# Kernel optimization log

Hardware: AMD Instinct MI355X
Metric: run time of the kernel (lower is better)

The kernel has to match this reference:

```python
import jax, jax.numpy as jnp
import numpy as np
import math

D_MODEL = 1024
NUM_HEADS = 16
D_HEAD = D_MODEL // NUM_HEADS          # 64
N_FREQ = D_HEAD // 2 + 1               # 33 rfft bins
COMPRESSION_RATIO = 0.5


def setup_inputs() -> dict:
    key = jax.random.key(0)
    k_x, k_qkv, k_out, k_b, k_m = jax.random.split(key, 5)
    B, S = 2, 2048
    x = jax.random.normal(k_x, (B, S, D_MODEL), dtype=jnp.float32)
    # Linear weights stored as [in, out] (torch Linear uses [out, in]; math identical).
    w_qkv = jax.random.normal(k_qkv, (D_MODEL, 3 * D_MODEL), dtype=jnp.float32) / math.sqrt(D_MODEL)
    w_out = jax.random.normal(k_out, (D_MODEL, D_MODEL), dtype=jnp.float32) / math.sqrt(D_MODEL)
    b_out = jax.random.normal(k_b, (D_MODEL,), dtype=jnp.float32) * 0.01
    # Learned per-frequency-bin mask logits of AdaptiveFrequencyMask(d_state=d_head).
    # Initialized around logit(compression_ratio) with small noise.
    init_logit = math.log(COMPRESSION_RATIO / (1.0 - COMPRESSION_RATIO))
    mask_logits = init_logit + 0.1 * jax.random.normal(k_m, (N_FREQ,), dtype=jnp.float32)
    return {"x": x, "w_qkv": w_qkv, "w_out": w_out, "b_out": b_out, "mask_logits": mask_logits}


def _spectral_filter(t, mask):
    # rfft over d_head dim, apply learned soft mask, inverse rfft.  t: [B,H,S,dh]
    tf = jnp.fft.rfft(t, axis=-1)          # [B,H,S,N_FREQ] complex
    tf = tf * mask                          # broadcast real mask over bins
    return jnp.fft.irfft(tf, n=t.shape[-1], axis=-1).astype(t.dtype)


def reference(x, w_qkv, w_out, b_out, mask_logits):
    B, S, D = x.shape
    H, dh = NUM_HEADS, D_HEAD
    qkv = x @ w_qkv                                         # [B,S,3D]
    q, k, v = jnp.split(qkv, 3, axis=-1)
    # [B,S,D] -> [B,H,S,dh]
    to_heads = lambda t: t.reshape(B, S, H, dh).transpose(0, 2, 1, 3)
    q, k, v = to_heads(q), to_heads(k), to_heads(v)
    mask = jax.nn.sigmoid(mask_logits)                      # [N_FREQ]
    q = _spectral_filter(q, mask)
    k = _spectral_filter(k, mask)
    scores = jnp.einsum('bhqd,bhkd->bhqk', q, k) / math.sqrt(dh)
    attn = jax.nn.softmax(scores, axis=-1)                  # dropout p=0 (eval)
    out = jnp.einsum('bhqk,bhkd->bhqd', attn, v)
    out = out.transpose(0, 2, 1, 3).reshape(B, S, D)
    return out @ w_out + b_out
```

## Files before the change

kernel.cpp:

```cpp
#include <hip/hip_runtime.h>

#define S_LEN 2048
#define NH    16
#define DH    64
#define DM    1024
#define NQKV  3072

typedef __attribute__((ext_vector_type(8))) __bf16 bf16x8;
typedef __attribute__((ext_vector_type(4))) float  f32x4;
typedef unsigned short ushort_t;

static __device__ __forceinline__ unsigned short bf16b(float f) {
  return __builtin_bit_cast(unsigned short, (__bf16)f);
}

static __device__ __forceinline__ float exp2v(float x) {
  return __builtin_amdgcn_exp2f(x);
}

static __device__ __forceinline__ bf16x8 pack8(float4 f0, float4 f1) {
  uint4 v;
  v.x = ((unsigned)bf16b(f0.y) << 16) | bf16b(f0.x);
  v.y = ((unsigned)bf16b(f0.w) << 16) | bf16b(f0.z);
  v.z = ((unsigned)bf16b(f1.y) << 16) | bf16b(f1.x);
  v.w = ((unsigned)bf16b(f1.w) << 16) | bf16b(f1.z);
  return __builtin_bit_cast(bf16x8, v);
}

static __device__ __forceinline__ void glds16(const void* g, void* l) {
  __builtin_amdgcn_global_load_lds((const __attribute__((address_space(1))) unsigned int*)g,
                                   (__attribute__((address_space(3))) unsigned int*)l, 16, 0, 0);
}

#define OFF_WT  65536ull
#define OFF_WOT 6356992ull
#define OFF_Q   8454144ull
#define OFF_K   16842752ull
#define OFF_V   25231360ull
#define OFF_AO  33619968ull

__global__ __launch_bounds__(256) void k_fold(const float* __restrict__ wqkv,
                                              const float* __restrict__ logits,
                                              unsigned short* __restrict__ Wt) {
  __shared__ float msk[33];
  __shared__ float Kd[64];
  __shared__ __align__(16) unsigned short Fb[64][72];
  int t = threadIdx.x;
  if (t < 33) msk[t] = 1.0f / (1.0f + __expf(-logits[t]));
  __syncthreads();
  if (t < 64) {
    float acc = msk[0];
    #pragma unroll
    for (int f = 1; f < 32; ++f) {
      int r = (f * t) & 63;
      acc += 2.0f * msk[f] * __cosf((float)r * (6.28318530717958647692f / 64.0f));
    }
    acc += msk[32] * ((t & 1) ? -1.0f : 1.0f);
    Kd[t] = acc * (1.0f / 64.0f);
  }
  __syncthreads();
  for (int idx = t; idx < 4096; idx += 256) {
    int j = idx >> 6, i = idx & 63;
    Fb[j][i] = bf16b(Kd[(j - i) & 63]);
  }
  __syncthreads();

  int lane = t & 63, w = t >> 6;
  int m16 = lane & 15, quad = lane >> 4;
  int kx = blockIdx.x, yy = blockIdx.y;
  int which = yy >> 4, h = yy & 15;
  int base = which * 1024 + h * 64;

  bf16x8 af0 = *(const bf16x8*)(&Fb[w * 16 + m16][quad * 8]);
  bf16x8 af1 = *(const bf16x8*)(&Fb[w * 16 + m16][32 + quad * 8]);

  f32x4 acc[8] = {};
  #pragma unroll 2
  for (int n = 0; n < 8; ++n) {
    const float* Wg = wqkv + (size_t)(kx * 128 + n * 16 + m16) * NQKV + base + quad * 8;
    float4 a0 = *(const float4*)(Wg);
    float4 a1 = *(const float4*)(Wg + 4);
    float4 b0 = *(const float4*)(Wg + 32);
    float4 b1 = *(const float4*)(Wg + 36);
    acc[n] = __builtin_amdgcn_mfma_f32_16x16x32_bf16(af0, pack8(a0, a1), acc[n], 0, 0, 0);
    acc[n] = __builtin_amdgcn_mfma_f32_16x16x32_bf16(af1, pack8(b0, b1), acc[n], 0, 0, 0);
  }
  float sc = (which == 0) ? 0.18033688011112042f : 1.0f;
  #pragma unroll
  for (int n = 0; n < 8; ++n) {
    #pragma unroll
    for (int r = 0; r < 4; ++r) {
      int j = w * 16 + quad * 4 + r;
      Wt[(size_t)(base + j) * DM + kx * 128 + n * 16 + m16] = bf16b(acc[n][r] * sc);
    }
  }
}

__global__ __launch_bounds__(256) void k_transpose(const float* __restrict__ wqkv,
                                                   const float* __restrict__ wout,
                                                   unsigned short* __restrict__ Wt,
                                                   unsigned short* __restrict__ Wot) {
  __shared__ float Ts[64][65];
  int bid = blockIdx.x;
  int t = threadIdx.x;
  if (bid < 256) {
    int kt = bid & 15, nt = bid >> 4;
    int cb = 2048 + nt * 64, kbase = kt * 64;
    #pragma unroll
    for (int p = 0; p < 16; ++p) {
      int kk = p * 4 + (t >> 6);
      Ts[kk][t & 63] = wqkv[(size_t)(kbase + kk) * NQKV + cb + (t & 63)];
    }
    __syncthreads();
    #pragma unroll
    for (int p = 0; p < 16; ++p) {
      int nn = p * 4 + (t >> 6);
      Wt[(size_t)(cb + nn) * DM + kbase + (t & 63)] = bf16b(Ts[t & 63][nn]);
    }
  } else {
    int b2 = bid - 256;
    int kt = b2 & 15, nt = b2 >> 4;
    int cb = nt * 64, kbase = kt * 64;
    #pragma unroll
    for (int p = 0; p < 16; ++p) {
      int kk = p * 4 + (t >> 6);
      Ts[kk][t & 63] = wout[(size_t)(kbase + kk) * DM + cb + (t & 63)];
    }
    __syncthreads();
    #pragma unroll
    for (int p = 0; p < 16; ++p) {
      int nn = p * 4 + (t >> 6);
      Wot[(size_t)(cb + nn) * DM + kbase + (t & 63)] = bf16b(Ts[t & 63][nn]);
    }
  }
}

__global__ __launch_bounds__(256) void k_castx(const float* __restrict__ x,
                                               unsigned short* __restrict__ xb) {
  size_t i = ((size_t)blockIdx.x * 256 + threadIdx.x) * 8;
  const float4* xp = (const float4*)(x + i);
  float4 a = xp[0], b = xp[1];
  uint4 v;
  v.x = ((unsigned)bf16b(a.y) << 16) | bf16b(a.x);
  v.y = ((unsigned)bf16b(a.w) << 16) | bf16b(a.z);
  v.z = ((unsigned)bf16b(b.y) << 16) | bf16b(b.x);
  v.w = ((unsigned)bf16b(b.w) << 16) | bf16b(b.z);
  *(uint4*)(xb + i) = v;
}

__device__ __forceinline__ void gemm_core_async(const unsigned short* __restrict__ A,
                                                const unsigned short* __restrict__ Bw,
                                                int bm, int bn, unsigned short* smem,
                                                f32x4 (&acc)[4][4]) {
  unsigned short* As = smem;
  unsigned short* Bs = smem + 8192;
  int t = threadIdx.x, lane = t & 63, w = t >> 6;
  int m16 = lane & 15, quad = lane >> 4;
  int wr = (w >> 1) * 64, wc = (w & 1) * 64;
  int lr = lane >> 3, lc = lane & 7;
  int gc = lc ^ lr;
  int xr = m16 & 7;
  const unsigned short* Agb = A  + (size_t)(bm * 128) * DM + gc * 8;
  const unsigned short* Bgb = Bw + (size_t)(bn * 128) * DM + gc * 8;

  for (int k0 = 0; k0 < DM; k0 += 64) {
    #pragma unroll
    for (int p = 0; p < 4; ++p) {
      int row = p * 32 + w * 8 + lr;
      glds16(Agb + (size_t)row * DM + k0, As + row * 64 + lc * 8);
      glds16(Bgb + (size_t)row * DM + k0, Bs + row * 64 + lc * 8);
    }
    __syncthreads();
    #pragma unroll
    for (int kk = 0; kk < 2; ++kk) {
      bf16x8 af[4], bfr[4];
      #pragma unroll
      for (int i = 0; i < 4; ++i)
        af[i] = *(const bf16x8*)(As + (wr + i * 16 + m16) * 64 + ((kk * 4 + quad) ^ xr) * 8);
      #pragma unroll
      for (int j = 0; j < 4; ++j)
        bfr[j] = *(const bf16x8*)(Bs + (wc + j * 16 + m16) * 64 + ((kk * 4 + quad) ^ xr) * 8);
      #pragma unroll
      for (int i = 0; i < 4; ++i)
        #pragma unroll
        for (int j = 0; j < 4; ++j)
          acc[i][j] = __builtin_amdgcn_mfma_f32_16x16x32_bf16(af[i], bfr[j], acc[i][j], 0, 0, 0);
    }
    __syncthreads();
  }
}

__global__ __launch_bounds__(256) void k_gemm_qkv(const unsigned short* __restrict__ xb,
                                                  const unsigned short* __restrict__ Bw,
                                                  unsigned short* __restrict__ Qb,
                                                  unsigned short* __restrict__ Kb,
                                                  unsigned short* __restrict__ Vt) {
  __shared__ __align__(16) unsigned short smem[18432];
  f32x4 acc[4][4] = {};
  int bn = blockIdx.x, bm = blockIdx.y;
  gemm_core_async(xb, Bw, bm, bn, smem, acc);

  int t = threadIdx.x, lane = t & 63, w = t >> 6;
  int m16 = lane & 15, quad = lane >> 4;
  int wr = (w >> 1) * 64, wc = (w & 1) * 64;
  int b = bm >> 4, srow = (bm & 15) * 128;
  int which = bn >> 3;
  ushort_t (*Tr)[130] = (ushort_t(*)[130])smem;
  if (which < 2) {
    #pragma unroll
    for (int i = 0; i < 4; ++i)
      #pragma unroll
      for (int j = 0; j < 4; ++j)
        #pragma unroll
        for (int r = 0; r < 4; ++r)
          Tr[wr + i * 16 + quad * 4 + r][wc + j * 16 + m16] = bf16b(acc[i][j][r]);
    __syncthreads();
    int row = t >> 1, half = t & 1;
    int cloc = bn * 128 + half * 64 - which * 1024;
    int h = cloc >> 6;
    unsigned short* dst = (which ? Kb : Qb) +
        ((size_t)(b * 16 + h) * 2048 + srow + row) * 64;
    #pragma unroll
    for (int p = 0; p < 8; ++p)
      *(uint4*)(dst + p * 8) = *(const uint4*)(&Tr[row][half * 64 + p * 8]);
  } else {
    #pragma unroll
    for (int i = 0; i < 4; ++i)
      #pragma unroll
      for (int j = 0; j < 4; ++j)
        #pragma unroll
        for (int r = 0; r < 4; ++r)
          Tr[wc + j * 16 + m16][wr + i * 16 + quad * 4 + r] = bf16b(acc[i][j][r]);
    __syncthreads();
    int dl = t >> 1, half = t & 1;
    int cloc = (bn - 16) * 128 + dl;
    int h = cloc >> 6, d = cloc & 63;
    unsigned short* dst = Vt + ((size_t)(b * 16 + h) * 64 + d) * 2048 + srow + half * 64;
    #pragma unroll
    for (int p = 0; p < 8; ++p)
      *(uint4*)(dst + p * 8) = *(const uint4*)(&Tr[dl][half * 64 + p * 8]);
  }
}

__global__ __launch_bounds__(256, 3) void k_attn(const unsigned short* __restrict__ Qb,
                                                 const unsigned short* __restrict__ Kb,
                                                 const unsigned short* __restrict__ Vt,
                                                 unsigned short* __restrict__ AO) {
  __shared__ __align__(16) unsigned short smem[25088];
  int t = threadIdx.x;
  int w = t >> 6, lane = t & 63;
  int m16 = lane & 15, quad = lane >> 4;
  int bid = blockIdx.x;
  int jj = bid >> 3;
  int bh = ((jj & 3) << 3) + (bid & 7);
  int qbase = (jj >> 2) * 128 + w * 32;

  const unsigned short* Qp = Qb + ((size_t)bh * S_LEN + qbase + m16) * DH + quad * 8;
  bf16x8 aq00 = *(const bf16x8*)(Qp);
  bf16x8 aq01 = *(const bf16x8*)(Qp + 32);
  bf16x8 aq10 = *(const bf16x8*)(Qp + 16 * DH);
  bf16x8 aq11 = *(const bf16x8*)(Qp + 16 * DH + 32);
  const unsigned short* Kbase = Kb + (size_t)bh * S_LEN * DH;
  const unsigned short* Vbase = Vt + (size_t)bh * DH * S_LEN;

  unsigned short* Pw = smem + 16384 + w * 2176;
  int xr = m16 & 7;

  int trow = t >> 3;
  int tcol = t & 7;
  int gswz = tcol ^ (trow & 7);

  f32x4 o0[4] = {}, o1[4] = {};
  float l0 = 0.f, l1 = 0.f;
  f32x4 zero = {0.f, 0.f, 0.f, 0.f};

  {
    const unsigned short* g;
    g = Kbase + (size_t)trow * 64 + gswz * 8;        glds16(g, smem + trow * 64 + tcol * 8);
    g = Kbase + (size_t)(trow + 32) * 64 + gswz * 8; glds16(g, smem + (trow + 32) * 64 + tcol * 8);
    g = Vbase + (size_t)trow * S_LEN + gswz * 8;        glds16(g, smem + 8192 + trow * 64 + tcol * 8);
    g = Vbase + (size_t)(trow + 32) * S_LEN + gswz * 8; glds16(g, smem + 8192 + (trow + 32) * 64 + tcol * 8);
  }
  __syncthreads();

  #pragma unroll 1
  for (int kt = 0; kt < S_LEN / 64; ++kt) {
    int cur = kt & 1, nxt = cur ^ 1;
    if (kt + 1 < S_LEN / 64) {
      int kk = (kt + 1) * 64;
      const unsigned short* g;
      g = Kbase + (size_t)(kk + trow) * 64 + gswz * 8;
      glds16(g, smem + nxt * 4096 + trow * 64 + tcol * 8);
      g = Kbase + (size_t)(kk + trow + 32) * 64 + gswz * 8;
      glds16(g, smem + nxt * 4096 + (trow + 32) * 64 + tcol * 8);
      g = Vbase + (size_t)trow * S_LEN + kk + gswz * 8;
      glds16(g, smem + 8192 + nxt * 4096 + trow * 64 + tcol * 8);
      g = Vbase + (size_t)(trow + 32) * S_LEN + kk + gswz * 8;
      glds16(g, smem + 8192 + nxt * 4096 + (trow + 32) * 64 + tcol * 8);
    }
    unsigned short* Ksh = smem + cur * 4096;
    unsigned short* Vsh = smem + 8192 + cur * 4096;

    f32x4 st0[4], st1[4];
    #pragma unroll
    for (int g = 0; g < 4; ++g) {
      int rk = g * 16 + m16;
      bf16x8 kf0 = *(const bf16x8*)(Ksh + rk * 64 + ((quad ^ xr) * 8));
      bf16x8 kf1 = *(const bf16x8*)(Ksh + rk * 64 + (((4 + quad) ^ xr) * 8));
      st0[g] = __builtin_amdgcn_mfma_f32_16x16x32_bf16(kf0, aq00, zero, 0, 0, 0);
      st0[g] = __builtin_amdgcn_mfma_f32_16x16x32_bf16(kf1, aq01, st0[g], 0, 0, 0);
      st1[g] = __builtin_amdgcn_mfma_f32_16x16x32_bf16(kf0, aq10, zero, 0, 0, 0);
      st1[g] = __builtin_amdgcn_mfma_f32_16x16x32_bf16(kf1, aq11, st1[g], 0, 0, 0);
    }
    #pragma unroll
    for (int g = 0; g < 4; ++g) {
      float p0 = exp2v(st0[g][0]), p1 = exp2v(st0[g][1]);
      float p2 = exp2v(st0[g][2]), p3 = exp2v(st0[g][3]);
      l0 += (p0 + p1) + (p2 + p3);
      uint2 pk;
      pk.x = ((unsigned)bf16b(p1) << 16) | bf16b(p0);
      pk.y = ((unsigned)bf16b(p3) << 16) | bf16b(p2);
      *(uint2*)(Pw + m16 * 68 + g * 16 + quad * 4) = pk;
    }
    #pragma unroll
    for (int g = 0; g < 4; ++g) {
      float p0 = exp2v(st1[g][0]), p1 = exp2v(st1[g][1]);
      float p2 = exp2v(st1[g][2]), p3 = exp2v(st1[g][3]);
      l1 += (p0 + p1) + (p2 + p3);
      uint2 pk;
      pk.x = ((unsigned)bf16b(p1) << 16) | bf16b(p0);
      pk.y = ((unsigned)bf16b(p3) << 16) | bf16b(p2);
      *(uint2*)(Pw + (16 + m16) * 68 + g * 16 + quad * 4) = pk;
    }
    #pragma unroll
    for (int c = 0; c < 2; ++c) {
      bf16x8 ap0 = *(const bf16x8*)(Pw + m16 * 68 + c * 32 + quad * 8);
      bf16x8 ap1 = *(const bf16x8*)(Pw + (16 + m16) * 68 + c * 32 + quad * 8);
      #pragma unroll
      for (int j = 0; j < 4; ++j) {
        int dv = j * 16 + m16;
        bf16x8 bv = *(const bf16x8*)(Vsh + dv * 64 + (((c * 4 + quad) ^ xr) * 8));
        o0[j] = __builtin_amdgcn_mfma_f32_16x16x32_bf16(ap0, bv, o0[j], 0, 0, 0);
        o1[j] = __builtin_amdgcn_mfma_f32_16x16x32_bf16(ap1, bv, o1[j], 0, 0, 0);
      }
    }
    __syncthreads();
  }

  l0 += __shfl_xor(l0, 16); l0 += __shfl_xor(l0, 32);
  l1 += __shfl_xor(l1, 16); l1 += __shfl_xor(l1, 32);
  float i0 = 1.0f / l0, i1 = 1.0f / l1;
  int b = bh >> 4, h = bh & 15;
  #pragma unroll
  for (int r = 0; r < 4; ++r) {
    float v0 = __shfl(i0, quad * 4 + r);
    float v1 = __shfl(i1, quad * 4 + r);
    size_t row0 = (size_t)b * S_LEN + qbase + quad * 4 + r;
    unsigned short* d0 = AO + row0 * DM + h * DH + m16;
    unsigned short* d1 = d0 + (size_t)16 * DM;
    #pragma unroll
    for (int j = 0; j < 4; ++j) {
      d0[j * 16] = bf16b(o0[j][r] * v0);
      d1[j * 16] = bf16b(o1[j][r] * v1);
    }
  }
}

__global__ __launch_bounds__(256) void k_gemm_out(const unsigned short* __restrict__ A,
                                                  const unsigned short* __restrict__ Bw,
                                                  const float* __restrict__ bias,
                                                  float* __restrict__ out) {
  __shared__ __align__(16) unsigned short smem[18432];
  f32x4 acc[4][4] = {};
  int bn = blockIdx.x, bm = blockIdx.y;
  gemm_core_async(A, Bw, bm, bn, smem, acc);

  int t = threadIdx.x, lane = t & 63, w = t >> 6;
  int m16 = lane & 15, quad = lane >> 4;
  int wr = (w >> 1) * 64, wc = (w & 1) * 64;
  #pragma unroll
  for (int i = 0; i < 4; ++i) {
    int grow = bm * 128 + wr + i * 16 + quad * 4;
    #pragma unroll
    for (int j = 0; j < 4; ++j) {
      int gc = bn * 128 + wc + j * 16 + m16;
      float bb = bias[gc];
      #pragma unroll
      for (int r = 0; r < 4; ++r)
        out[(size_t)(grow + r) * DM + gc] = acc[i][j][r] + bb;
    }
  }
}

extern "C" void kernel_launch(void* const* d_in, const int* in_sizes, int n_in,
                              void* d_out, int out_size, void* d_ws, size_t ws_size,
                              hipStream_t stream) {
  const float* x    = (const float*)d_in[0];
  const float* wqkv = (const float*)d_in[1];
  const float* wout = (const float*)d_in[2];
  const float* bout = (const float*)d_in[3];
  const float* mlog = (const float*)d_in[4];
  char* ws = (char*)d_ws;
  unsigned short* Wt  = (unsigned short*)(ws + OFF_WT);
  unsigned short* Wot = (unsigned short*)(ws + OFF_WOT);
  unsigned short* Qb  = (unsigned short*)(ws + OFF_Q);
  unsigned short* Kb  = (unsigned short*)(ws + OFF_K);
  unsigned short* Vt  = (unsigned short*)(ws + OFF_V);
  unsigned short* xb  = (unsigned short*)(ws + OFF_AO);
  unsigned short* AO  = (unsigned short*)(ws + OFF_AO);
  float* out = (float*)d_out;

  k_fold<<<dim3(8, 32), dim3(256), 0, stream>>>(wqkv, mlog, Wt);
  k_transpose<<<dim3(512), dim3(256), 0, stream>>>(wqkv, wout, Wt, Wot);
  k_castx<<<dim3(2048), dim3(256), 0, stream>>>(x, xb);
  k_gemm_qkv<<<dim3(24, 32), dim3(256), 0, stream>>>(xb, Wt, Qb, Kb, Vt);
  k_attn<<<dim3(512), dim3(256), 0, stream>>>(Qb, Kb, Vt, AO);
  k_gemm_out<<<dim3(8, 32), dim3(256), 0, stream>>>(AO, Wot, bout, out);
}
```

Baseline: 226.8 us.

## Fuse prep kernels and split attention waves to 16 query rows each

Merges the mask-fold, weight transpose and x cast kernels into a single launch, removing two kernel launches. The attention kernel moves to 512-thread blocks where each of eight waves handles 16 query rows instead of 32, lowering per-wave registers to raise occupancy and halving per-thread K/V tile load work. The trade-off is more LDS fragment reads per MFMA since each K/V fragment is reused across fewer query rows per wave.

```diff
diff --git a/kernel.cpp b/kernel.cpp
--- a/kernel.cpp
+++ b/kernel.cpp
@@ -39,113 +39,113 @@
 #define OFF_V   25231360ull
 #define OFF_AO  33619968ull
 
-__global__ __launch_bounds__(256) void k_fold(const float* __restrict__ wqkv,
+__global__ __launch_bounds__(256) void k_prep(const float* __restrict__ wqkv,
+                                              const float* __restrict__ wout,
+                                              const float* __restrict__ x,
                                               const float* __restrict__ logits,
-                                              unsigned short* __restrict__ Wt) {
-  __shared__ float msk[33];
-  __shared__ float Kd[64];
-  __shared__ __align__(16) unsigned short Fb[64][72];
-  int t = threadIdx.x;
-  if (t < 33) msk[t] = 1.0f / (1.0f + __expf(-logits[t]));
-  __syncthreads();
-  if (t < 64) {
-    float acc = msk[0];
-    #pragma unroll
-    for (int f = 1; f < 32; ++f) {
-      int r = (f * t) & 63;
-      acc += 2.0f * msk[f] * __cosf((float)r * (6.28318530717958647692f / 64.0f));
-    }
-    acc += msk[32] * ((t & 1) ? -1.0f : 1.0f);
-    Kd[t] = acc * (1.0f / 64.0f);
-  }
-  __syncthreads();
-  for (int idx = t; idx < 4096; idx += 256) {
-    int j = idx >> 6, i = idx & 63;
-    Fb[j][i] = bf16b(Kd[(j - i) & 63]);
-  }
-  __syncthreads();
-
-  int lane = t & 63, w = t >> 6;
-  int m16 = lane & 15, quad = lane >> 4;
-  int kx = blockIdx.x, yy = blockIdx.y;
-  int which = yy >> 4, h = yy & 15;
-  int base = which * 1024 + h * 64;
-
-  bf16x8 af0 = *(const bf16x8*)(&Fb[w * 16 + m16][quad * 8]);
-  bf16x8 af1 = *(const bf16x8*)(&Fb[w * 16 + m16][32 + quad * 8]);
-
-  f32x4 acc[8] = {};
-  #pragma unroll 2
-  for (int n = 0; n < 8; ++n) {
-    const float* Wg = wqkv + (size_t)(kx * 128 + n * 16 + m16) * NQKV + base + quad * 8;
-    float4 a0 = *(const float4*)(Wg);
-    float4 a1 = *(const float4*)(Wg + 4);
-    float4 b0 = *(const float4*)(Wg + 32);
-    float4 b1 = *(const float4*)(Wg + 36);
-    acc[n] = __builtin_amdgcn_mfma_f32_16x16x32_bf16(af0, pack8(a0, a1), acc[n], 0, 0, 0);
-    acc[n] = __builtin_amdgcn_mfma_f32_16x16x32_bf16(af1, pack8(b0, b1), acc[n], 0, 0, 0);
-  }
-  float sc = (which == 0) ? 0.18033688011112042f : 1.0f;
-  #pragma unroll
-  for (int n = 0; n < 8; ++n) {
-    #pragma unroll
-    for (int r = 0; r < 4; ++r) {
-      int j = w * 16 + quad * 4 + r;
-      Wt[(size_t)(base + j) * DM + kx * 128 + n * 16 + m16] = bf16b(acc[n][r] * sc);
-    }
-  }
-}
-
-__global__ __launch_bounds__(256) void k_transpose(const float* __restrict__ wqkv,
-                                                   const float* __restrict__ wout,
-                                                   unsigned short* __restrict__ Wt,
-                                                   unsigned short* __restrict__ Wot) {
-  __shared__ float Ts[64][65];
+                                              unsigned short* __restrict__ Wt,
+                                              unsigned short* __restrict__ Wot,
+                                              unsigned short* __restrict__ xb) {
+  __shared__ __align__(16) char sbuf[16640];
   int bid = blockIdx.x;
   int t = threadIdx.x;
+
   if (bid < 256) {
-    int kt = bid & 15, nt = bid >> 4;
-    int cb = 2048 + nt * 64, kbase = kt * 64;
-    #pragma unroll
-    for (int p = 0; p < 16; ++p) {
-      int kk = p * 4 + (t >> 6);
-      Ts[kk][t & 63] = wqkv[(size_t)(kbase + kk) * NQKV + cb + (t & 63)];
-    }
-    __syncthreads();
-    #pragma unroll
-    for (int p = 0; p < 16; ++p) {
-      int nn = p * 4 + (t >> 6);
-      Wt[(size_t)(cb + nn) * DM + kbase + (t & 63)] = bf16b(Ts[t & 63][nn]);
+    float* msk = (float*)sbuf;
+    float* Kd  = (float*)(sbuf + 144);
+    ushort_t (*Fb)[72] = (ushort_t(*)[72])(sbuf + 416);
+    if (t < 33) msk[t] = 1.0f / (1.0f + __expf(-logits[t]));
+    __syncthreads();
+    if (t < 64) {
+      float acc = msk[0];
+      #pragma unroll
+      for (int f = 1; f < 32; ++f) {
+        int r = (f * t) & 63;
+        acc += 2.0f * msk[f] * __cosf((float)r * (6.28318530717958647692f / 64.0f));
+      }
+      acc += msk[32] * ((t & 1) ? -1.0f : 1.0f);
+      Kd[t] = acc * (1.0f / 64.0f);
+    }
+    __syncthreads();
+    for (int idx = t; idx < 4096; idx += 256) {
+      int j = idx >> 6, i = idx & 63;
+      Fb[j][i] = bf16b(Kd[(j - i) & 63]);
+    }
+    __syncthreads();
+
+    int lane = t & 63, w = t >> 6;
+    int m16 = lane & 15, quad = lane >> 4;
+    int kx = bid >> 5, yy = bid & 31;
+    int which = yy >> 4, h = yy & 15;
+    int base = which * 1024 + h * 64;
+
+    bf16x8 af0 = *(const bf16x8*)(&Fb[w * 16 + m16][quad * 8]);
+    bf16x8 af1 = *(const bf16x8*)(&Fb[w * 16 + m16][32 + quad * 8]);
+
+    f32x4 acc[8] = {};
+    #pragma unroll 2
+    for (int n = 0; n < 8; ++n) {
+      const float* Wg = wqkv + (size_t)(kx * 128 + n * 16 + m16) * NQKV + base + quad * 8;
+      float4 a0 = *(const float4*)(Wg);
+      float4 a1 = *(const float4*)(Wg + 4);
+      float4 b0 = *(const float4*)(Wg + 32);
+      float4 b1 = *(const float4*)(Wg + 36);
+      acc[n] = __builtin_amdgcn_mfma_f32_16x16x32_bf16(af0, pack8(a0, a1), acc[n], 0, 0, 0);
+      acc[n] = __builtin_amdgcn_mfma_f32_16x16x32_bf16(af1, pack8(b0, b1), acc[n], 0, 0, 0);
+    }
+    float sc = (which == 0) ? 0.18033688011112042f : 1.0f;
+    #pragma unroll
+    for (int n = 0; n < 8; ++n) {
+      #pragma unroll
+      for (int r = 0; r < 4; ++r) {
+        int j = w * 16 + quad * 4 + r;
+        Wt[(size_t)(base + j) * DM + kx * 128 + n * 16 + m16] = bf16b(acc[n][r] * sc);
+      }
+    }
+  } else if (bid < 768) {
+    float (*Ts)[65] = (float(*)[65])sbuf;
+    int b1 = bid - 256;
+    if (b1 < 256) {
+      int kt = b1 & 15, nt = b1 >> 4;
+      int cb = 2048 + nt * 64, kbase = kt * 64;
+      #pragma unroll
+      for (int p = 0; p < 16; ++p) {
+        int kk = p * 4 + (t >> 6);
+        Ts[kk][t & 63] = wqkv[(size_t)(kbase + kk) * NQKV + cb + (t & 63)];
+      }
+      __syncthreads();
+      #pragma unroll
+      for (int p = 0; p < 16; ++p) {
+        int nn = p * 4 + (t >> 6);
+        Wt[(size_t)(cb + nn) * DM + kbase + (t & 63)] = bf16b(Ts[t & 63][nn]);
+      }
+    } else {
+      int b2 = b1 - 256;
+      int kt = b2 & 15, nt = b2 >> 4;
+      int cb = nt * 64, kbase = kt * 64;
+      #pragma unroll
+      for (int p = 0; p < 16; ++p) {
+        int kk = p * 4 + (t >> 6);
+        Ts[kk][t & 63] = wout[(size_t)(kbase + kk) * DM + cb + (t & 63)];
+      }
+      __syncthreads();
+      #pragma unroll
+      for (int p = 0; p < 16; ++p) {
+        int nn = p * 4 + (t >> 6);
+        Wot[(size_t)(cb + nn) * DM + kbase + (t & 63)] = bf16b(Ts[t & 63][nn]);
+      }
     }
   } else {
-    int b2 = bid - 256;
-    int kt = b2 & 15, nt = b2 >> 4;
-    int cb = nt * 64, kbase = kt * 64;
-    #pragma unroll
-    for (int p = 0; p < 16; ++p) {
-      int kk = p * 4 + (t >> 6);
-      Ts[kk][t & 63] = wout[(size_t)(kbase + kk) * DM + cb + (t & 63)];
-    }
-    __syncthreads();
-    #pragma unroll
-    for (int p = 0; p < 16; ++p) {
-      int nn = p * 4 + (t >> 6);
-      Wot[(size_t)(cb + nn) * DM + kbase + (t & 63)] = bf16b(Ts[t & 63][nn]);
-    }
-  }
-}
-
-__global__ __launch_bounds__(256) void k_castx(const float* __restrict__ x,
-                                               unsigned short* __restrict__ xb) {
-  size_t i = ((size_t)blockIdx.x * 256 + threadIdx.x) * 8;
-  const float4* xp = (const float4*)(x + i);
-  float4 a = xp[0], b = xp[1];
-  uint4 v;
-  v.x = ((unsigned)bf16b(a.y) << 16) | bf16b(a.x);
-  v.y = ((unsigned)bf16b(a.w) << 16) | bf16b(a.z);
-  v.z = ((unsigned)bf16b(b.y) << 16) | bf16b(b.x);
-  v.w = ((unsigned)bf16b(b.w) << 16) | bf16b(b.z);
-  *(uint4*)(xb + i) = v;
+    size_t i = ((size_t)(bid - 768) * 256 + t) * 8;
+    const float4* xp = (const float4*)(x + i);
+    float4 a = xp[0], b = xp[1];
+    uint4 v;
+    v.x = ((unsigned)bf16b(a.y) << 16) | bf16b(a.x);
+    v.y = ((unsigned)bf16b(a.w) << 16) | bf16b(a.z);
+    v.z = ((unsigned)bf16b(b.y) << 16) | bf16b(b.x);
+    v.w = ((unsigned)bf16b(b.w) << 16) | bf16b(b.z);
+    *(uint4*)(xb + i) = v;
+  }
 }
 
 __device__ __forceinline__ void gemm_core_async(const unsigned short* __restrict__ A,
@@ -242,7 +242,7 @@
   }
 }
 
-__global__ __launch_bounds__(256, 3) void k_attn(const unsigned short* __restrict__ Qb,
+__global__ __launch_bounds__(512, 4) void k_attn(const unsigned short* __restrict__ Qb,
                                                  const unsigned short* __restrict__ Kb,
                                                  const unsigned short* __restrict__ Vt,
                                                  unsigned short* __restrict__ AO) {
@@ -253,34 +253,27 @@
   int bid = blockIdx.x;
   int jj = bid >> 3;
   int bh = ((jj & 3) << 3) + (bid & 7);
-  int qbase = (jj >> 2) * 128 + w * 32;
+  int qbase = (jj >> 2) * 128 + w * 16;
 
   const unsigned short* Qp = Qb + ((size_t)bh * S_LEN + qbase + m16) * DH + quad * 8;
-  bf16x8 aq00 = *(const bf16x8*)(Qp);
-  bf16x8 aq01 = *(const bf16x8*)(Qp + 32);
-  bf16x8 aq10 = *(const bf16x8*)(Qp + 16 * DH);
-  bf16x8 aq11 = *(const bf16x8*)(Qp + 16 * DH + 32);
+  bf16x8 aq0 = *(const bf16x8*)(Qp);
+  bf16x8 aq1 = *(const bf16x8*)(Qp + 32);
   const unsigned short* Kbase = Kb + (size_t)bh * S_LEN * DH;
   const unsigned short* Vbase = Vt + (size_t)bh * DH * S_LEN;
 
-  unsigned short* Pw = smem + 16384 + w * 2176;
+  unsigned short* Pw = smem + 16384 + w * 1088;
   int xr = m16 & 7;
 
   int trow = t >> 3;
   int tcol = t & 7;
   int gswz = tcol ^ (trow & 7);
 
-  f32x4 o0[4] = {}, o1[4] = {};
-  float l0 = 0.f, l1 = 0.f;
+  f32x4 o[4] = {};
+  float l = 0.f;
   f32x4 zero = {0.f, 0.f, 0.f, 0.f};
 
-  {
-    const unsigned short* g;
-    g = Kbase + (size_t)trow * 64 + gswz * 8;        glds16(g, smem + trow * 64 + tcol * 8);
-    g = Kbase + (size_t)(trow + 32) * 64 + gswz * 8; glds16(g, smem + (trow + 32) * 64 + tcol * 8);
-    g = Vbase + (size_t)trow * S_LEN + gswz * 8;        glds16(g, smem + 8192 + trow * 64 + tcol * 8);
-    g = Vbase + (size_t)(trow + 32) * S_LEN + gswz * 8; glds16(g, smem + 8192 + (trow + 32) * 64 + tcol * 8);
-  }
+  glds16(Kbase + (size_t)trow * 64 + gswz * 8,    smem + trow * 64 + tcol * 8);
+  glds16(Vbase + (size_t)trow * S_LEN + gswz * 8, smem + 8192 + trow * 64 + tcol * 8);
   __syncthreads();
 
   #pragma unroll 1
@@ -288,81 +281,57 @@
     int cur = kt & 1, nxt = cur ^ 1;
     if (kt + 1 < S_LEN / 64) {
       int kk = (kt + 1) * 64;
-      const unsigned short* g;
-      g = Kbase + (size_t)(kk + trow) * 64 + gswz * 8;
-      glds16(g, smem + nxt * 4096 + trow * 64 + tcol * 8);
-      g = Kbase + (size_t)(kk + trow + 32) * 64 + gswz * 8;
-      glds16(g, smem + nxt * 4096 + (trow + 32) * 64 + tcol * 8);
-      g = Vbase + (size_t)trow * S_LEN + kk + gswz * 8;
-      glds16(g, smem + 8192 + nxt * 4096 + trow * 64 + tcol * 8);
-      g = Vbase + (size_t)(trow + 32) * S_LEN + kk + gswz * 8;
-      glds16(g, smem + 8192 + nxt * 4096 + (trow + 32) * 64 + tcol * 8);
+      glds16(Kbase + (size_t)(kk + trow) * 64 + gswz * 8,
+             smem + nxt * 4096 + trow * 64 + tcol * 8);
+      glds16(Vbase + (size_t)trow * S_LEN + kk + gswz * 8,
+             smem + 8192 + nxt * 4096 + trow * 64 + tcol * 8);
     }
     unsigned short* Ksh = smem + cur * 4096;
     unsigned short* Vsh = smem + 8192 + cur * 4096;
 
-    f32x4 st0[4], st1[4];
+    f32x4 st[4];
     #pragma unroll
     for (int g = 0; g < 4; ++g) {
       int rk = g * 16 + m16;
       bf16x8 kf0 = *(const bf16x8*)(Ksh + rk * 64 + ((quad ^ xr) * 8));
       bf16x8 kf1 = *(const bf16x8*)(Ksh + rk * 64 + (((4 + quad) ^ xr) * 8));
-      st0[g] = __builtin_amdgcn_mfma_f32_16x16x32_bf16(kf0, aq00, zero, 0, 0, 0);
-      st0[g] = __builtin_amdgcn_mfma_f32_16x16x32_bf16(kf1, aq01, st0[g], 0, 0, 0);
-      st1[g] = __builtin_amdgcn_mfma_f32_16x16x32_bf16(kf0, aq10, zero, 0, 0, 0);
-      st1[g] = __builtin_amdgcn_mfma_f32_16x16x32_bf16(kf1, aq11, st1[g], 0, 0, 0);
+      st[g] = __builtin_amdgcn_mfma_f32_16x16x32_bf16(kf0, aq0, zero, 0, 0, 0);
+      st[g] = __builtin_amdgcn_mfma_f32_16x16x32_bf16(kf1, aq1, st[g], 0, 0, 0);
     }
     #pragma unroll
     for (int g = 0; g < 4; ++g) {
-      float p0 = exp2v(st0[g][0]), p1 = exp2v(st0[g][1]);
-      float p2 = exp2v(st0[g][2]), p3 = exp2v(st0[g][3]);
-      l0 += (p0 + p1) + (p2 + p3);
+      float p0 = exp2v(st[g][0]), p1 = exp2v(st[g][1]);
+      float p2 = exp2v(st[g][2]), p3 = exp2v(st[g][3]);
+      l += (p0 + p1) + (p2 + p3);
       uint2 pk;
       pk.x = ((unsigned)bf16b(p1) << 16) | bf16b(p0);
       pk.y = ((unsigned)bf16b(p3) << 16) | bf16b(p2);
       *(uint2*)(Pw + m16 * 68 + g * 16 + quad * 4) = pk;
     }
     #pragma unroll
-    for (int g = 0; g < 4; ++g) {
-      float p0 = exp2v(st1[g][0]), p1 = exp2v(st1[g][1]);
-      float p2 = exp2v(st1[g][2]), p3 = exp2v(st1[g][3]);
-      l1 += (p0 + p1) + (p2 + p3);
-      uint2 pk;
-      pk.x = ((unsigned)bf16b(p1) << 16) | bf16b(p0);
-      pk.y = ((unsigned)bf16b(p3) << 16) | bf16b(p2);
-      *(uint2*)(Pw + (16 + m16) * 68 + g * 16 + quad * 4) = pk;
-    }
-    #pragma unroll
     for (int c = 0; c < 2; ++c) {
-      bf16x8 ap0 = *(const bf16x8*)(Pw + m16 * 68 + c * 32 + quad * 8);
-      bf16x8 ap1 = *(const bf16x8*)(Pw + (16 + m16) * 68 + c * 32 + quad * 8);
+      bf16x8 ap = *(const bf16x8*)(Pw + m16 * 68 + c * 32 + quad * 8);
       #pragma unroll
       for (int j = 0; j < 4; ++j) {
         int dv = j * 16 + m16;
         bf16x8 bv = *(const bf16x8*)(Vsh + dv * 64 + (((c * 4 + quad) ^ xr) * 8));
-        o0[j] = __builtin_amdgcn_mfma_f32_16x16x32_bf16(ap0, bv, o0[j], 0, 0, 0);
-        o1[j] = __builtin_amdgcn_mfma_f32_16x16x32_bf16(ap1, bv, o1[j], 0, 0, 0);
-      }
-    }
-    __syncthreads();
-  }
-
-  l0 += __shfl_xor(l0, 16); l0 += __shfl_xor(l0, 32);
-  l1 += __shfl_xor(l1, 16); l1 += __shfl_xor(l1, 32);
-  float i0 = 1.0f / l0, i1 = 1.0f / l1;
+        o[j] = __builtin_amdgcn_mfma_f32_16x16x32_bf16(ap, bv, o[j], 0, 0, 0);
+      }
+    }
+    __syncthreads();
+  }
+
+  l += __shfl_xor(l, 16); l += __shfl_xor(l, 32);
+  float iv = 1.0f / l;
   int b = bh >> 4, h = bh & 15;
   #pragma unroll
   for (int r = 0; r < 4; ++r) {
-    float v0 = __shfl(i0, quad * 4 + r);
-    float v1 = __shfl(i1, quad * 4 + r);
+    float v0 = __shfl(iv, quad * 4 + r);
     size_t row0 = (size_t)b * S_LEN + qbase + quad * 4 + r;
     unsigned short* d0 = AO + row0 * DM + h * DH + m16;
-    unsigned short* d1 = d0 + (size_t)16 * DM;
-    #pragma unroll
-    for (int j = 0; j < 4; ++j) {
-      d0[j * 16] = bf16b(o0[j][r] * v0);
-      d1[j * 16] = bf16b(o1[j][r] * v1);
-    }
+    #pragma unroll
+    for (int j = 0; j < 4; ++j)
+      d0[j * 16] = bf16b(o[j][r] * v0);
   }
 }
 
@@ -410,10 +379,8 @@
   unsigned short* AO  = (unsigned short*)(ws + OFF_AO);
   float* out = (float*)d_out;
 
-  k_fold<<<dim3(8, 32), dim3(256), 0, stream>>>(wqkv, mlog, Wt);
-  k_transpose<<<dim3(512), dim3(256), 0, stream>>>(wqkv, wout, Wt, Wot);
-  k_castx<<<dim3(2048), dim3(256), 0, stream>>>(x, xb);
+  k_prep<<<dim3(2816), dim3(256), 0, stream>>>(wqkv, wout, x, mlog, Wt, Wot, xb);
   k_gemm_qkv<<<dim3(24, 32), dim3(256), 0, stream>>>(xb, Wt, Qb, Kb, Vt);
-  k_attn<<<dim3(512), dim3(256), 0, stream>>>(Qb, Kb, Vt, AO);
+  k_attn<<<dim3(512), dim3(512), 0, stream>>>(Qb, Kb, Vt, AO);
   k_gemm_out<<<dim3(8, 32), dim3(256), 0, stream>>>(AO, Wot, bout, out);
 }
```

Measured after the change: 215.8 us. -4.9%, faster.
